# Performance work log

Hardware: AMD Instinct MI355X
Metric: run time of the kernel (lower is better)

## Reference

```python
import jax, jax.numpy as jnp
import numpy as np

BN_EPS = 1e-5


def conv1x1(x, w, b):
    # x: [B,C,H,W], w: [O,C], b: [O]
    return jnp.einsum('bchw,oc->bohw', x, w) + b[None, :, None, None]


def dwconv3(x, w, b):
    # depthwise 3x3, SAME padding; w: [C,1,3,3]
    y = jax.lax.conv_general_dilated(
        x, w, window_strides=(1, 1), padding='SAME',
        feature_group_count=x.shape[1],
        dimension_numbers=('NCHW', 'OIHW', 'NCHW'))
    return y + b[None, :, None, None]


def setup_inputs() -> dict:
    key = jax.random.key(0)
    B, C, H, W, E = 8, 256, 80, 80, 2
    ks = jax.random.split(key, 16)

    def n(k, shape, sc=0.02):
        return jax.random.normal(k, shape, dtype=jnp.float32) * sc

    return {
        'x': jax.random.normal(ks[0], (B, C, H, W), dtype=jnp.float32),
        # BatchNorm2d (inference: running stats + affine)
        'bn_gamma': jnp.ones((C,), jnp.float32),
        'bn_beta': jnp.zeros((C,), jnp.float32),
        'bn_mean': n(ks[1], (C,), 0.1),
        'bn_var': jnp.abs(n(ks[2], (C,), 0.5)) + 1.0,
        # SpectralGating complex per-channel gate
        'alpha_real': n(ks[3], (1, C, 1, 1), 0.1),
        'alpha_imag': n(ks[4], (1, C, 1, 1), 0.1),
        # LocalMamba2D (fallback path)
        'pi_w': n(ks[5], (C, C)), 'pi_b': jnp.zeros((C,), jnp.float32),
        'dw_w': n(ks[6], (C, 1, 3, 3)), 'dw_b': jnp.zeros((C,), jnp.float32),
        'fpw_w': n(ks[7], (C, C)), 'fpw_b': jnp.zeros((C,), jnp.float32),
        'ffn1_w': n(ks[8], (C * E, C)), 'ffn1_b': jnp.zeros((C * E,), jnp.float32),
        'ffn2_w': n(ks[9], (C, C * E)), 'ffn2_b': jnp.zeros((C,), jnp.float32),
        'po_w': n(ks[10], (C, C)), 'po_b': jnp.zeros((C,), jnp.float32),
        # post 1x1 conv
        'post_w': n(ks[11], (C, C)), 'post_b': jnp.zeros((C,), jnp.float32),
    }


def reference(x, bn_gamma, bn_beta, bn_mean, bn_var, alpha_real, alpha_imag,
              pi_w, pi_b, dw_w, dw_b, fpw_w, fpw_b,
              ffn1_w, ffn1_b, ffn2_w, ffn2_b, po_w, po_b,
              post_w, post_b):
    res = x
    # pre_norm: BatchNorm2d in inference mode
    inv = jax.lax.rsqrt(bn_var + BN_EPS)
    h = (x - bn_mean[None, :, None, None]) * (bn_gamma * inv)[None, :, None, None] \
        + bn_beta[None, :, None, None]
    # SpectralGating: rfft2 (ortho) -> complex per-channel gate -> irfft2
    H, W = h.shape[2], h.shape[3]
    X = jnp.fft.rfft2(h, norm='ortho')              # [B,C,H,W//2+1] complex
    Y = X * (alpha_real + 1j * alpha_imag)
    h = jnp.fft.irfft2(Y, s=(H, W), norm='ortho')
    # LocalMamba2D fallback: proj_in -> dw3x3 -> GELU -> 1x1 -> FFN -> proj_out (+res)
    # H,W are multiples of window=8, so pad branch is a no-op.
    res2 = h
    t = conv1x1(h, pi_w, pi_b)
    y = jax.nn.gelu(dwconv3(t, dw_w, dw_b), approximate=False)
    y = conv1x1(y, fpw_w, fpw_b)
    y = jax.nn.gelu(conv1x1(y, ffn1_w, ffn1_b), approximate=False)
    y = conv1x1(y, ffn2_w, ffn2_b)
    h = conv1x1(y, po_w, po_b) + res2
    # post 1x1 conv + outer residual
    out = conv1x1(h, post_w, post_b)
    return out + res
```

## Files before the change

kernel.cpp:

```cpp
#include <hip/hip_runtime.h>
#include <cmath>

#define BB 8
#define CC 256
#define HH 80
#define WW 80
#define HWSZ 6400
#define PLANE_FLOATS (CC * HWSZ)
#define TENSOR_FLOATS (BB * PLANE_FLOATS)

using short8v = __attribute__((ext_vector_type(8))) short;
using f32x4  = __attribute__((ext_vector_type(4))) float;

__device__ __forceinline__ float gelu_exact(float v) {
    return 0.5f * v * (1.0f + erff(v * 0.70710678118654752440f));
}

__device__ __forceinline__ unsigned short f2bf(float f) {
    unsigned int u = __float_as_uint(f);
    unsigned int r = (u + 0x7FFFu + ((u >> 16) & 1u)) >> 16;
    return (unsigned short)r;
}
__device__ __forceinline__ float bf2f(unsigned short h) {
    return __uint_as_float(((unsigned int)h) << 16);
}

struct PreAll {
    const float* src[7];
    int stride[7];
    int runs[7];
    int dstOff[7];
};

__global__ __launch_bounds__(256)
void preconvert_kernel(PreAll d, unsigned short* __restrict__ packH,
                       unsigned short* __restrict__ packL)
{
    const int m = blockIdx.y;
    const int r = blockIdx.x * 256 + threadIdx.x;
    if (r >= d.runs[m]) return;
    const int ks = r >> 10;
    const int rem = r & 1023;
    const int fi = rem >> 6;
    const int l = rem & 63;
    const int o = fi * 16 + (l & 15);
    const int c0 = ks * 32 + ((l >> 4)) * 8;
    const float* src = d.src[m] + (size_t)o * d.stride[m] + c0;
    short8v hv, lv;
#pragma unroll
    for (int j = 0; j < 8; ++j) {
        const float v = src[j];
        const unsigned short h = f2bf(v);
        const unsigned short lo = f2bf(v - bf2f(h));
        hv[j] = (short)h; lv[j] = (short)lo;
    }
    *(short8v*)(packH + d.dstOff[m] + (size_t)r * 8) = hv;
    *(short8v*)(packL + d.dstOff[m] + (size_t)r * 8) = lv;
}

struct GTab { float g[40]; };

__global__ __launch_bounds__(256)
void bn_gate_kernel(const float* __restrict__ x,
                    const float* __restrict__ gamma, const float* __restrict__ beta,
                    const float* __restrict__ mean,  const float* __restrict__ var,
                    const float* __restrict__ ar,    const float* __restrict__ ai,
                    float* __restrict__ out, GTab gt)
{
    __shared__ float sv[HWSZ];
    const int blk = blockIdx.x;
    const int c = blk & (CC - 1);
    const float sc = gamma[c] * rsqrtf(var[c] + 1e-5f);
    const float sh = beta[c] - mean[c] * sc;
    const float a = ar[c], bgate = ai[c];
    const size_t base = (size_t)blk * HWSZ;

    const float4* x4 = (const float4*)(x + base);
    float4* s4 = (float4*)sv;
    for (int i = threadIdx.x; i < HWSZ / 4; i += 256) {
        float4 v = x4[i];
        v.x = fmaf(sc, v.x, sh); v.y = fmaf(sc, v.y, sh);
        v.z = fmaf(sc, v.z, sh); v.w = fmaf(sc, v.w, sh);
        s4[i] = v;
    }
    __syncthreads();

#pragma unroll 1
    for (int r = 0; r < 4; ++r) {
        const int gi = r * 256 + threadIdx.x;
        if (gi >= 800) break;
        const int y = gi / 10;
        const int x0 = (gi - y * 10) * 8;
        const float* row = sv + y * WW;

        float rbuf[88];
#pragma unroll
        for (int q = 0; q < 22; ++q) {
            int col = x0 + 4 * q;
            if (col >= 80) col -= 80;
            const float4 v = *(const float4*)&row[col];
            rbuf[4 * q + 0] = v.x; rbuf[4 * q + 1] = v.y;
            rbuf[4 * q + 2] = v.z; rbuf[4 * q + 3] = v.w;
        }
        float outv[8];
#pragma unroll
        for (int e = 0; e < 8; ++e) {
            float acc = 0.0f;
#pragma unroll
            for (int jj = 0; jj < 40; ++jj) {
                const int j = 2 * jj + 1;
                acc = fmaf(gt.g[jj], rbuf[80 + e - j], acc);
            }
            outv[e] = fmaf(a, rbuf[80 + e], bgate * acc);
        }
        float4 o0 = {outv[0], outv[1], outv[2], outv[3]};
        float4 o1 = {outv[4], outv[5], outv[6], outv[7]};
        *(float4*)&out[base + (size_t)y * WW + x0]     = o0;
        *(float4*)&out[base + (size_t)y * WW + x0 + 4] = o1;
    }
}

template <int EPI, int KS>
__global__ __launch_bounds__(256)
void gemm_mfma(const float* __restrict__ X, const float* __restrict__ X2,
               const unsigned short* __restrict__ Wh,
               const unsigned short* __restrict__ Wl,
               const float* __restrict__ bias,
               const float* __restrict__ res, float* __restrict__ Y)
{
    __shared__ short8v sB[2][2][256];

    const int bz = blockIdx.z;
    const int nBase = blockIdx.x * 64;
    const int t = threadIdx.x;
    const int l = t & 63;
    const int w = t >> 6;

    const float* Xb  = X + (size_t)bz * PLANE_FLOATS + nBase;
    const float* X2b = (KS == 16) ? (X2 + (size_t)bz * PLANE_FLOATS + nBase) : nullptr;
    float* Yb = Y + (size_t)bz * PLANE_FLOATS;

    const int sn = t & 63;
    const int scg = t >> 6;
    const int slot = ((sn >> 4) * 64) + scg * 16 + (sn & 15);

    f32x4 acc[4][4];
#pragma unroll
    for (int m = 0; m < 4; ++m)
#pragma unroll
        for (int n2 = 0; n2 < 4; ++n2) acc[m][n2] = (f32x4){0.f, 0.f, 0.f, 0.f};

    float xv[8];
#pragma unroll
    for (int j = 0; j < 8; ++j)
        xv[j] = Xb[(size_t)(scg * 8 + j) * HWSZ + sn];

    short8v ah[4], al[4];
    {
        const size_t fb = ((size_t)(w * 4) * 64 + l) * 8;
#pragma unroll
        for (int m = 0; m < 4; ++m) {
            ah[m] = *(const short8v*)(Wh + fb + (size_t)m * 512);
            al[m] = *(const short8v*)(Wl + fb + (size_t)m * 512);
        }
    }
    {
        short8v hv, lv;
#pragma unroll
        for (int j = 0; j < 8; ++j) {
            const unsigned short h = f2bf(xv[j]);
            const unsigned short lo = f2bf(xv[j] - bf2f(h));
            hv[j] = (short)h; lv[j] = (short)lo;
        }
        sB[0][0][slot] = hv; sB[0][1][slot] = lv;
    }
    __syncthreads();

#pragma unroll
    for (int ks = 0; ks < KS; ++ks) {
        const int p = ks & 1;
        float xv2[8];
        if (ks < KS - 1) {
            const int kn = ks + 1;
            const float* src = (KS == 16 && kn >= 8) ? X2b : Xb;
            const int kk = (KS == 16 && kn >= 8) ? kn - 8 : kn;
#pragma unroll
            for (int j = 0; j < 8; ++j)
                xv2[j] = src[(size_t)(kk * 32 + scg * 8 + j) * HWSZ + sn];
        }
        short8v bh[4], bl[4];
#pragma unroll
        for (int n2 = 0; n2 < 4; ++n2) {
            bh[n2] = sB[p][0][n2 * 64 + l];
            bl[n2] = sB[p][1][n2 * 64 + l];
        }
        short8v ah2[4], al2[4];
        if (ks < KS - 1) {
            const size_t fb = ((size_t)((ks + 1) * 16 + w * 4) * 64 + l) * 8;
#pragma unroll
            for (int m = 0; m < 4; ++m) {
                ah2[m] = *(const short8v*)(Wh + fb + (size_t)m * 512);
                al2[m] = *(const short8v*)(Wl + fb + (size_t)m * 512);
            }
        }
#pragma unroll
        for (int m = 0; m < 4; ++m)
#pragma unroll
            for (int n2 = 0; n2 < 4; ++n2) {
                acc[m][n2] = __builtin_amdgcn_mfma_f32_16x16x32_bf16(
                    ah[m], bh[n2], acc[m][n2], 0, 0, 0);
                acc[m][n2] = __builtin_amdgcn_mfma_f32_16x16x32_bf16(
                    ah[m], bl[n2], acc[m][n2], 0, 0, 0);
                acc[m][n2] = __builtin_amdgcn_mfma_f32_16x16x32_bf16(
                    al[m], bh[n2], acc[m][n2], 0, 0, 0);
            }
        if (ks < KS - 1) {
            short8v hv, lv;
#pragma unroll
            for (int j = 0; j < 8; ++j) {
                const unsigned short h = f2bf(xv2[j]);
                const unsigned short lo = f2bf(xv2[j] - bf2f(h));
                hv[j] = (short)h; lv[j] = (short)lo;
            }
            sB[p ^ 1][0][slot] = hv; sB[p ^ 1][1][slot] = lv;
            __syncthreads();
#pragma unroll
            for (int m = 0; m < 4; ++m) { ah[m] = ah2[m]; al[m] = al2[m]; }
        }
    }

    const int col = l & 15, g = l >> 4;
#pragma unroll
    for (int m = 0; m < 4; ++m) {
        const int o0 = w * 64 + m * 16 + g * 4;
#pragma unroll
        for (int r = 0; r < 4; ++r) {
            const int o = o0 + r;
            const float bo = bias[o];
            float* yrow = Yb + (size_t)o * HWSZ + nBase;
            const float* rrow = (EPI == 2)
                ? (res + ((size_t)bz * CC + o) * HWSZ + nBase) : nullptr;
#pragma unroll
            for (int n2 = 0; n2 < 4; ++n2) {
                const int n = n2 * 16 + col;
                float v = acc[m][n2][r] + bo;
                if (EPI == 1) v = gelu_exact(v);
                if (EPI == 2) v += rrow[n];
                yrow[n] = v;
            }
        }
    }
}

__global__ __launch_bounds__(256)
void dwconv_gelu_kernel(const float* __restrict__ in, const float* __restrict__ w,
                        const float* __restrict__ bias, float* __restrict__ out)
{
    const int g = blockIdx.x * 256 + threadIdx.x;
    const int plane = g / 1600;
    const int pg = g - plane * 1600;
    const int c = plane & (CC - 1);
    const int y = pg / 20;
    const int x0 = (pg - y * 20) * 4;
    const float* p = in + (size_t)plane * HWSZ;

    float rb[3][12];
#pragma unroll
    for (int ky = 0; ky < 3; ++ky) {
        const int yy = y + ky - 1;
        const bool yok = (yy >= 0) && (yy < HH);
        const float* prow = p + yy * WW;
#pragma unroll
        for (int q = 0; q < 3; ++q) {
            const int cx = x0 + 4 * q - 4;
            float4 v = {0.f, 0.f, 0.f, 0.f};
            if (yok && cx >= 0 && cx < WW) v = *(const float4*)&prow[cx];
            rb[ky][4 * q + 0] = v.x; rb[ky][4 * q + 1] = v.y;
            rb[ky][4 * q + 2] = v.z; rb[ky][4 * q + 3] = v.w;
        }
    }
    const float* wc = w + c * 9;
    float wv[9];
#pragma unroll
    for (int k = 0; k < 9; ++k) wv[k] = wc[k];
    const float bo = bias[c];

    float4 res;
    float* rp = (float*)&res;
#pragma unroll
    for (int e = 0; e < 4; ++e) {
        float s = bo;
#pragma unroll
        for (int ky = 0; ky < 3; ++ky)
#pragma unroll
            for (int kx = 0; kx < 3; ++kx)
                s = fmaf(wv[ky * 3 + kx], rb[ky][e + kx + 3], s);
        rp[e] = gelu_exact(s);
    }
    *(float4*)&out[(size_t)plane * HWSZ + (size_t)y * WW + x0] = res;
}

extern "C" void kernel_launch(void* const* d_in, const int* in_sizes, int n_in,
                              void* d_out, int out_size, void* d_ws, size_t ws_size,
                              hipStream_t stream)
{
    const float* x        = (const float*)d_in[0];
    const float* bn_gamma = (const float*)d_in[1];
    const float* bn_beta  = (const float*)d_in[2];
    const float* bn_mean  = (const float*)d_in[3];
    const float* bn_var   = (const float*)d_in[4];
    const float* alpha_r  = (const float*)d_in[5];
    const float* alpha_i  = (const float*)d_in[6];
    const float* pi_w     = (const float*)d_in[7];
    const float* pi_b     = (const float*)d_in[8];
    const float* dw_w     = (const float*)d_in[9];
    const float* dw_b     = (const float*)d_in[10];
    const float* fpw_w    = (const float*)d_in[11];
    const float* fpw_b    = (const float*)d_in[12];
    const float* ffn1_w   = (const float*)d_in[13];
    const float* ffn1_b   = (const float*)d_in[14];
    const float* ffn2_w   = (const float*)d_in[15];
    const float* ffn2_b   = (const float*)d_in[16];
    const float* po_w     = (const float*)d_in[17];
    const float* po_b     = (const float*)d_in[18];
    const float* post_w   = (const float*)d_in[19];
    const float* post_b   = (const float*)d_in[20];

    float* bufA = (float*)d_ws;
    float* bufB = bufA + TENSOR_FLOATS;
    float* bufC = bufB + TENSOR_FLOATS;
    float* bufD = (float*)d_out;
    unsigned short* packH = (unsigned short*)(bufC + TENSOR_FLOATS);
    unsigned short* packL = packH + 524288;

    GTab gt;
    for (int jj = 0; jj < 40; ++jj) {
        const int j = 2 * jj + 1;
        double s = 0.0;
        for (int k = 1; k <= 39; ++k)
            s += sin(2.0 * 3.14159265358979323846 * (double)k * (double)j / 80.0);
        gt.g[jj] = (float)(-s / 40.0);
    }

    PreAll pd;
    pd.src[0] = pi_w;              pd.stride[0] = 256; pd.runs[0] = 8192;  pd.dstOff[0] = 0;
    pd.src[1] = fpw_w;             pd.stride[1] = 256; pd.runs[1] = 8192;  pd.dstOff[1] = 65536;
    pd.src[2] = ffn1_w;            pd.stride[2] = 256; pd.runs[2] = 8192;  pd.dstOff[2] = 131072;
    pd.src[3] = ffn1_w + 256*256;  pd.stride[3] = 256; pd.runs[3] = 8192;  pd.dstOff[3] = 196608;
    pd.src[4] = ffn2_w;            pd.stride[4] = 512; pd.runs[4] = 16384; pd.dstOff[4] = 262144;
    pd.src[5] = po_w;              pd.stride[5] = 256; pd.runs[5] = 8192;  pd.dstOff[5] = 393216;
    pd.src[6] = post_w;            pd.stride[6] = 256; pd.runs[6] = 8192;  pd.dstOff[6] = 458752;

    const dim3 gGrid(HWSZ / 64, 1, BB);
    const dim3 gBlk(256);

    preconvert_kernel<<<dim3(64, 7), 256, 0, stream>>>(pd, packH, packL);
    bn_gate_kernel<<<BB * CC, 256, 0, stream>>>(x, bn_gamma, bn_beta, bn_mean,
                                                bn_var, alpha_r, alpha_i, bufA, gt);
    gemm_mfma<0, 8><<<gGrid, gBlk, 0, stream>>>(bufA, nullptr, packH, packL,
                                                pi_b, nullptr, bufB);
    dwconv_gelu_kernel<<<TENSOR_FLOATS / 1024, 256, 0, stream>>>(bufB, dw_w, dw_b, bufC);
    gemm_mfma<0, 8><<<gGrid, gBlk, 0, stream>>>(bufC, nullptr, packH + 65536,
                                                packL + 65536, fpw_b, nullptr, bufB);
    gemm_mfma<1, 8><<<gGrid, gBlk, 0, stream>>>(bufB, nullptr, packH + 131072,
                                                packL + 131072, ffn1_b, nullptr, bufC);
    gemm_mfma<1, 8><<<gGrid, gBlk, 0, stream>>>(bufB, nullptr, packH + 196608,
                                                packL + 196608, ffn1_b + 256, nullptr, bufD);
    gemm_mfma<0, 16><<<gGrid, gBlk, 0, stream>>>(bufC, bufD, packH + 262144,
                                                 packL + 262144, ffn2_b, nullptr, bufB);
    gemm_mfma<2, 8><<<gGrid, gBlk, 0, stream>>>(bufB, nullptr, packH + 393216,
                                                packL + 393216, po_b, bufA, bufC);
    gemm_mfma<2, 8><<<gGrid, gBlk, 0, stream>>>(bufC, nullptr, packH + 458752,
                                                packL + 458752, post_b, x, (float*)d_out);
}
```

Baseline: 426.3 us.

## Fold proj_out and post conv into one K=512 GEMM; deepen input prefetch

```diff
diff --git a/kernel.cpp b/kernel.cpp
--- a/kernel.cpp
+++ b/kernel.cpp
@@ -23,6 +23,30 @@
 }
 __device__ __forceinline__ float bf2f(unsigned short h) {
     return __uint_as_float(((unsigned int)h) << 16);
+}
+
+__global__ __launch_bounds__(256)
+void combine_po_post(const float* __restrict__ po_w, const float* __restrict__ po_b,
+                     const float* __restrict__ post_w, const float* __restrict__ post_b,
+                     float* __restrict__ Wcomb, float* __restrict__ bcomb)
+{
+    __shared__ float red[256];
+    const int o = blockIdx.x;
+    const int c = threadIdx.x;
+    const float* prow = post_w + (size_t)o * 256;
+    float s = 0.f;
+#pragma unroll 4
+    for (int m = 0; m < 256; ++m)
+        s = fmaf(prow[m], po_w[(size_t)m * 256 + c], s);
+    Wcomb[(size_t)o * 512 + c] = s;
+    Wcomb[(size_t)o * 512 + 256 + c] = prow[c];
+    red[c] = prow[c] * po_b[c];
+    __syncthreads();
+    for (int st = 128; st > 0; st >>= 1) {
+        if (c < st) red[c] += red[c + st];
+        __syncthreads();
+    }
+    if (c == 0) bcomb[o] = red[0] + post_b[o];
 }
 
 struct PreAll {
@@ -150,11 +174,6 @@
 #pragma unroll
         for (int n2 = 0; n2 < 4; ++n2) acc[m][n2] = (f32x4){0.f, 0.f, 0.f, 0.f};
 
-    float xv[8];
-#pragma unroll
-    for (int j = 0; j < 8; ++j)
-        xv[j] = Xb[(size_t)(scg * 8 + j) * HWSZ + sn];
-
     short8v ah[4], al[4];
     {
         const size_t fb = ((size_t)(w * 4) * 64 + l) * 8;
@@ -164,12 +183,23 @@
             al[m] = *(const short8v*)(Wl + fb + (size_t)m * 512);
         }
     }
+    float xbuf[3][8];
+#pragma unroll
+    for (int d = 0; d < 3; ++d) {
+        if (d < KS) {
+            const float* src = (KS == 16 && d >= 8) ? X2b : Xb;
+            const int kk = (KS == 16 && d >= 8) ? d - 8 : d;
+#pragma unroll
+            for (int j = 0; j < 8; ++j)
+                xbuf[d][j] = src[(size_t)(kk * 32 + scg * 8 + j) * HWSZ + sn];
+        }
+    }
     {
         short8v hv, lv;
 #pragma unroll
         for (int j = 0; j < 8; ++j) {
-            const unsigned short h = f2bf(xv[j]);
-            const unsigned short lo = f2bf(xv[j] - bf2f(h));
+            const unsigned short h = f2bf(xbuf[0][j]);
+            const unsigned short lo = f2bf(xbuf[0][j] - bf2f(h));
             hv[j] = (short)h; lv[j] = (short)lo;
         }
         sB[0][0][slot] = hv; sB[0][1][slot] = lv;
@@ -179,15 +209,6 @@
 #pragma unroll
     for (int ks = 0; ks < KS; ++ks) {
         const int p = ks & 1;
-        float xv2[8];
-        if (ks < KS - 1) {
-            const int kn = ks + 1;
-            const float* src = (KS == 16 && kn >= 8) ? X2b : Xb;
-            const int kk = (KS == 16 && kn >= 8) ? kn - 8 : kn;
-#pragma unroll
-            for (int j = 0; j < 8; ++j)
-                xv2[j] = src[(size_t)(kk * 32 + scg * 8 + j) * HWSZ + sn];
-        }
         short8v bh[4], bl[4];
 #pragma unroll
         for (int n2 = 0; n2 < 4; ++n2) {
@@ -195,13 +216,21 @@
             bl[n2] = sB[p][1][n2 * 64 + l];
         }
         short8v ah2[4], al2[4];
-        if (ks < KS - 1) {
+        if (ks + 1 < KS) {
             const size_t fb = ((size_t)((ks + 1) * 16 + w * 4) * 64 + l) * 8;
 #pragma unroll
             for (int m = 0; m < 4; ++m) {
                 ah2[m] = *(const short8v*)(Wh + fb + (size_t)m * 512);
                 al2[m] = *(const short8v*)(Wl + fb + (size_t)m * 512);
             }
+        }
+        if (ks + 3 < KS) {
+            const int kn = ks + 3;
+            const float* src = (KS == 16 && kn >= 8) ? X2b : Xb;
+            const int kk = (KS == 16 && kn >= 8) ? kn - 8 : kn;
+#pragma unroll
+            for (int j = 0; j < 8; ++j)
+                xbuf[ks % 3][j] = src[(size_t)(kk * 32 + scg * 8 + j) * HWSZ + sn];
         }
 #pragma unroll
         for (int m = 0; m < 4; ++m)
@@ -214,12 +243,13 @@
                 acc[m][n2] = __builtin_amdgcn_mfma_f32_16x16x32_bf16(
                     al[m], bh[n2], acc[m][n2], 0, 0, 0);
             }
-        if (ks < KS - 1) {
+        if (ks + 1 < KS) {
             short8v hv, lv;
 #pragma unroll
             for (int j = 0; j < 8; ++j) {
-                const unsigned short h = f2bf(xv2[j]);
-                const unsigned short lo = f2bf(xv2[j] - bf2f(h));
+                const float v = xbuf[(ks + 1) % 3][j];
+                const unsigned short h = f2bf(v);
+                const unsigned short lo = f2bf(v - bf2f(h));
                 hv[j] = (short)h; lv[j] = (short)lo;
             }
             sB[p ^ 1][0][slot] = hv; sB[p ^ 1][1][slot] = lv;
@@ -332,6 +362,8 @@
     float* bufD = (float*)d_out;
     unsigned short* packH = (unsigned short*)(bufC + TENSOR_FLOATS);
     unsigned short* packL = packH + 524288;
+    float* Wcomb = (float*)(packL + 524288);
+    float* bcomb = Wcomb + 131072;
 
     GTab gt;
     for (int jj = 0; jj < 40; ++jj) {
@@ -348,13 +380,14 @@
     pd.src[2] = ffn1_w;            pd.stride[2] = 256; pd.runs[2] = 8192;  pd.dstOff[2] = 131072;
     pd.src[3] = ffn1_w + 256*256;  pd.stride[3] = 256; pd.runs[3] = 8192;  pd.dstOff[3] = 196608;
     pd.src[4] = ffn2_w;            pd.stride[4] = 512; pd.runs[4] = 16384; pd.dstOff[4] = 262144;
-    pd.src[5] = po_w;              pd.stride[5] = 256; pd.runs[5] = 8192;  pd.dstOff[5] = 393216;
-    pd.src[6] = post_w;            pd.stride[6] = 256; pd.runs[6] = 8192;  pd.dstOff[6] = 458752;
+    pd.src[5] = Wcomb;             pd.stride[5] = 512; pd.runs[5] = 16384; pd.dstOff[5] = 393216;
+    pd.src[6] = pi_w;              pd.stride[6] = 256; pd.runs[6] = 0;     pd.dstOff[6] = 0;
 
     const dim3 gGrid(HWSZ / 64, 1, BB);
     const dim3 gBlk(256);
 
-    preconvert_kernel<<<dim3(64, 7), 256, 0, stream>>>(pd, packH, packL);
+    combine_po_post<<<256, 256, 0, stream>>>(po_w, po_b, post_w, post_b, Wcomb, bcomb);
+    preconvert_kernel<<<dim3(64, 6), 256, 0, stream>>>(pd, packH, packL);
     bn_gate_kernel<<<BB * CC, 256, 0, stream>>>(x, bn_gamma, bn_beta, bn_mean,
                                                 bn_var, alpha_r, alpha_i, bufA, gt);
     gemm_mfma<0, 8><<<gGrid, gBlk, 0, stream>>>(bufA, nullptr, packH, packL,
@@ -368,8 +401,6 @@
                                                 packL + 196608, ffn1_b + 256, nullptr, bufD);
     gemm_mfma<0, 16><<<gGrid, gBlk, 0, stream>>>(bufC, bufD, packH + 262144,
                                                  packL + 262144, ffn2_b, nullptr, bufB);
-    gemm_mfma<2, 8><<<gGrid, gBlk, 0, stream>>>(bufB, nullptr, packH + 393216,
-                                                packL + 393216, po_b, bufA, bufC);
-    gemm_mfma<2, 8><<<gGrid, gBlk, 0, stream>>>(bufC, nullptr, packH + 458752,
-                                                packL + 458752, post_b, x, (float*)d_out);
-}
+    gemm_mfma<2, 16><<<gGrid, gBlk, 0, stream>>>(bufB, bufA, packH + 393216,
+                                                 packL + 393216, bcomb, x, (float*)d_out);
+}
```

After: 468.8 us. 10.0% more time.
